# Performance work log

Measured on AMD Instinct MI355X. Metric: run time of the kernel, lower is better.

Reference implementation:

```python
import jax, jax.numpy as jnp
import numpy as np


def conv1x1(x, w, b):
    # x: (B,C,H,W), w: (Cout,Cin), b: (Cout,) -- 1x1 conv == channel matmul
    return jnp.einsum('bchw,oc->bohw', x, w) + b[None, :, None, None]


def spatial_gate(q_feat, k_feat, scale):
    # Faithful to: matmul over flattened (B*HW, C) x (C, B*HW), then
    # max over keys, mean over the batch axis, softmax over spatial dims.
    B, C, H, W = q_feat.shape
    q = q_feat.reshape(B, C, H * W).transpose(0, 2, 1).reshape(B * H * W, C)
    k = k_feat.reshape(B, C, H * W).transpose(1, 0, 2).reshape(C, B * H * W)
    s = (q @ k).reshape(B * H * W, B, H * W)          # (BHW, B, HW)
    m = jnp.mean(jnp.max(s, axis=-1), axis=-1)        # (BHW,)
    w = jax.nn.softmax(m.reshape(B, H * W) * scale, axis=-1)
    return w.reshape(B, 1, H, W)


def setup_inputs() -> dict:
    key = jax.random.key(0)
    ks = jax.random.split(key, 10)
    C = 256
    shp = (8, C, 32, 32)
    inp = {
        'x4': jax.random.normal(ks[0], shp, jnp.float32),
        'x3': jax.random.normal(ks[1], shp, jnp.float32),
        'wq': jax.random.normal(ks[2], (C, C), jnp.float32) * 0.02,
        'bq': jnp.zeros((C,), jnp.float32),
        'wk': jax.random.normal(ks[3], (C, C), jnp.float32) * 0.02,
        'bk': jnp.zeros((C,), jnp.float32),
        'wv': jax.random.normal(ks[4], (C, C), jnp.float32) * 0.02,
        'bv': jnp.zeros((C,), jnp.float32),
        'w128': jax.random.normal(ks[5], (128, C), jnp.float32) * 0.02,
        'b128': jnp.zeros((128,), jnp.float32),
    }
    return inp


def reference(x4, x3, wq, bq, wk, bk, wv, bv, w128, b128):
    C = x4.shape[1]
    scale = 1.0 / (C ** 0.5)
    # shared QKV 1x1 convs applied to both inputs
    aq = conv1x1(x4, wq, bq)
    ak = conv1x1(x4, wk, bk)
    av = conv1x1(x4, wv, bv)
    bq_f = conv1x1(x3, wq, bq)
    bk_f = conv1x1(x3, wk, bk)
    bv_f = conv1x1(x3, wv, bv)
    # four gating branches: self-self (a), self-self (b), cross a->b, cross b->a
    a_x4 = conv1x1(spatial_gate(aq, ak, scale) * av, w128, b128)
    b_x3 = conv1x1(spatial_gate(bq_f, bk_f, scale) * bv_f, w128, b128)
    x43 = conv1x1(spatial_gate(aq, bk_f, scale) * bv_f, w128, b128)
    x34 = conv1x1(spatial_gate(bq_f, ak, scale) * av, w128, b128)
    # cat order: [x34, a_x4] then [x43, b_x3]
    ab_cat = jnp.concatenate([x34, a_x4, x43, b_x3], axis=1)  # (B,512,H,W)
    # Block2D loop: block class undefined in source; surrogate = identity
    # (ab12 = concat of the two chunks == ab_cat), applied depth=4 times.
    ab12 = ab_cat
    ab12 = ab_cat * ab12
    ab_avg = jnp.mean(ab12, axis=(2, 3), keepdims=True)        # (B,512,1,1)
    ab = jax.nn.softmax(ab_avg, axis=-1)   # softmax over size-1 axis -> ones
    final = ab * ab_cat
    return final
```

## Files before the change

### kernel.cpp

```cpp
#include <hip/hip_runtime.h>

typedef unsigned short ushort_t;
typedef unsigned char uchar_t;
typedef __attribute__((ext_vector_type(8))) short bf16x8;
typedef __attribute__((ext_vector_type(4))) float f32x4;
typedef __attribute__((ext_vector_type(16))) float f32x16;
typedef __attribute__((ext_vector_type(8))) int v8i;

__device__ __forceinline__ unsigned short f2bf(float f) {
  union { float f; unsigned int u; } v; v.f = f;
  unsigned int r = v.u + 0x7FFFu + ((v.u >> 16) & 1u);
  return (unsigned short)(r >> 16);
}

__device__ __forceinline__ float bf2f(unsigned short u) {
  union { unsigned int i; float f; } v; v.i = ((unsigned int)u) << 16;
  return v.f;
}

__device__ __forceinline__ void gl_lds16(const void* gsrc, void* ldst) {
  __builtin_amdgcn_global_load_lds(
      (const __attribute__((address_space(1))) void*)gsrc,
      (__attribute__((address_space(3))) void*)ldst, 16, 0, 0);
}

__device__ __forceinline__ int frag_idx(int oc, int ci) {
  return (((oc>>4)*8 + (ci>>5))<<9) + ((((ci>>3)&3)*16 + (oc&15))<<3) + (ci&7);
}

__global__ __launch_bounds__(256) void k1_weights(
    const float* __restrict__ wq, const float* __restrict__ bq,
    const float* __restrict__ wk, const float* __restrict__ bk,
    const float* __restrict__ wv, const float* __restrict__ bv,
    const float* __restrict__ w128,
    ushort_t* __restrict__ Wf, float* __restrict__ bias_all)
{
  const int ci = threadIdx.x;
  const int oc = blockIdx.x;
  if (oc < 512) {
    const float v = (oc < 256) ? wq[oc*256 + ci] : wk[(oc-256)*256 + ci];
    Wf[frag_idx(oc, ci)] = f2bf(v);
    if (ci == 0) bias_all[oc] = (oc < 256) ? bq[oc] : bk[oc-256];
  } else {
    const int o = oc - 512;
    const float* wr = w128 + (size_t)o*256;
    float a = 0.f;
    for (int co = 0; co < 256; co++) a += wr[co] * wv[co*256 + ci];
    Wf[frag_idx(oc, ci)] = f2bf(a);
    if (ci == 0) {
      float s = 0.f;
      for (int co = 0; co < 256; co++) s += wr[co] * bv[co];
      bias_all[oc] = s;
    }
  }
}

__global__ __launch_bounds__(256) void k2_features(
    const float* __restrict__ x4, const float* __restrict__ x3,
    const ushort_t* __restrict__ Wf, const float* __restrict__ bias_all,
    uchar_t* __restrict__ Qf8, uchar_t* __restrict__ Kf8, float* __restrict__ V)
{
  __shared__ ushort_t Af[32*512];
  __shared__ ushort_t Wl[2][32*512];
  __shared__ ushort_t Lt[64*72];

  const int tid = threadIdx.x;
  const int w = tid >> 6, lane = tid & 63;
  const int mrow = lane & 15, quad = lane >> 4;
  const int ln31 = lane & 31, half = lane >> 5;

  const int px0 = blockIdx.x * 64;
  const int src = px0 >> 13, b = (px0 >> 10) & 7, hw0 = px0 & 1023;
  const float* xp = (src ? x3 : x4) + (size_t)b*262144;

  const int ot0 = blockIdx.y * 5;

  for (int kb = 0; kb < 8; kb++)
    gl_lds16(Wf + ((size_t)((ot0*4 + w)*8 + kb)<<9) + lane*8,
             &Wl[ot0&1][(w*8+kb)*512]);

  {
    const int hw = hw0 + w*16 + mrow;
    for (int kb = 0; kb < 8; kb++) {
      const int ch0 = kb*32 + quad*8;
      bf16x8 pk;
      #pragma unroll
      for (int j = 0; j < 8; j++)
        ((ushort_t*)&pk)[j] = f2bf(xp[(size_t)(ch0 + j)*1024 + hw]);
      *(bf16x8*)&Af[(w*8 + kb)*512 + lane*8] = pk;
    }
  }
  __syncthreads();

  for (int ot = ot0; ot < ot0 + 5; ot++) {
    const int nbuf = (ot+1) & 1, cbuf = ot & 1;
    if (ot + 1 < ot0 + 5) {
      for (int kb = 0; kb < 8; kb++)
        gl_lds16(Wf + ((size_t)(((ot+1)*4 + w)*8 + kb)<<9) + lane*8,
                 &Wl[nbuf][(w*8+kb)*512]);
      asm volatile("s_waitcnt vmcnt(32)" ::: "memory");
    } else {
      asm volatile("s_waitcnt vmcnt(0)" ::: "memory");
    }

    f32x4 acc[4];
    #pragma unroll
    for (int lg = 0; lg < 4; lg++) acc[lg] = (f32x4){0.f,0.f,0.f,0.f};
    #pragma unroll
    for (int kb = 0; kb < 8; kb++) {
      const bf16x8 a = *(const bf16x8*)&Wl[cbuf][(w*8 + kb)*512 + lane*8];
      #pragma unroll
      for (int lg = 0; lg < 4; lg++) {
        const bf16x8 bx = *(const bf16x8*)&Af[(lg*8 + kb)*512 + lane*8];
        acc[lg] = __builtin_amdgcn_mfma_f32_16x16x32_bf16(a, bx, acc[lg], 0, 0, 0);
      }
    }
    const int ocl = w*16 + quad*4;
    const float4 bias4 = *(const float4*)&bias_all[ot*64 + ocl];

    if (ot < 8) {
      __syncthreads();
      #pragma unroll
      for (int lg = 0; lg < 4; lg++) {
        const int px = lg*16 + mrow;
        ushort4 pk;
        pk.x = f2bf(acc[lg][0] + bias4.x);
        pk.y = f2bf(acc[lg][1] + bias4.y);
        pk.z = f2bf(acc[lg][2] + bias4.z);
        pk.w = f2bf(acc[lg][3] + bias4.w);
        *(ushort4*)&Lt[px*72 + ocl] = pk;
      }
      __syncthreads();
      const int g = w >> 1, e = w & 1;
      const int row = g*32 + ln31;
      const ushort_t* lp = &Lt[row*72 + e*32 + half*8];
      float fl[8], fh[8];
      #pragma unroll
      for (int j = 0; j < 8; j++) { fl[j] = bf2f(lp[j]); fh[j] = bf2f(lp[16+j]); }
      int w0 = __builtin_amdgcn_cvt_pk_fp8_f32(fl[0], fl[1], 0, 0);
      w0     = __builtin_amdgcn_cvt_pk_fp8_f32(fl[2], fl[3], w0, 1);
      int w1 = __builtin_amdgcn_cvt_pk_fp8_f32(fl[4], fl[5], 0, 0);
      w1     = __builtin_amdgcn_cvt_pk_fp8_f32(fl[6], fl[7], w1, 1);
      int w2 = __builtin_amdgcn_cvt_pk_fp8_f32(fh[0], fh[1], 0, 0);
      w2     = __builtin_amdgcn_cvt_pk_fp8_f32(fh[2], fh[3], w2, 1);
      int w3 = __builtin_amdgcn_cvt_pk_fp8_f32(fh[4], fh[5], 0, 0);
      w3     = __builtin_amdgcn_cvt_pk_fp8_f32(fh[6], fh[7], w3, 1);
      uchar_t* dst = (ot < 4) ? Qf8 : Kf8;
      const size_t chunk = (size_t)((px0>>5) + g)*8 + (ot&3)*2 + e;
      int4 pk4; pk4.x = w0; pk4.y = w1; pk4.z = w2; pk4.w = w3;
      *(int4*)(dst + (chunk<<10) + lane*16) = pk4;
    } else {
      const int ocv0 = (ot-8)*64 + ocl;
      float* vb = V + (((size_t)(src*8 + b)*128) << 10) + hw0;
      #pragma unroll
      for (int lg = 0; lg < 4; lg++) {
        vb[(size_t)(ocv0+0)*1024 + lg*16 + mrow] = acc[lg][0] + bias4.x;
        vb[(size_t)(ocv0+1)*1024 + lg*16 + mrow] = acc[lg][1] + bias4.y;
        vb[(size_t)(ocv0+2)*1024 + lg*16 + mrow] = acc[lg][2] + bias4.z;
        vb[(size_t)(ocv0+3)*1024 + lg*16 + mrow] = acc[lg][3] + bias4.w;
      }
    }
  }
}

__global__ __launch_bounds__(512, 2) void k3_smax(
    const uchar_t* __restrict__ Qf8, const uchar_t* __restrict__ Kf8,
    float* __restrict__ Pm)
{
  __shared__ __align__(16) uchar_t Kl[2][32768];

  const int tid = threadIdx.x;
  const int bt = blockIdx.x >> 5;
  const int rt = blockIdx.x & 31;
  const int w = tid >> 6, lane = tid & 63;
  const int ln31 = lane & 31, half = lane >> 5;

  const int rgb = rt*16 + w*2;
  const int ph = (blockIdx.x & 1)*4;

  #pragma unroll
  for (int q = 0; q < 4; q++) {
    const int c = w*4 + q;
    const int cg = bt*32 + ph*4 + (c>>3);
    gl_lds16(Kf8 + (((size_t)cg*8 + (c&7))<<10) + lane*16, &Kl[0][c*1024]);
  }

  v8i qa[2][4];
  #pragma unroll
  for (int rg = 0; rg < 2; rg++)
    #pragma unroll
    for (int u = 0; u < 4; u++) {
      const int4 p0 = *(const int4*)(Qf8 + (((size_t)(rgb + rg)*8 + 2*u+0)<<10) + lane*16);
      const int4 p1 = *(const int4*)(Qf8 + (((size_t)(rgb + rg)*8 + 2*u+1)<<10) + lane*16);
      qa[rg][u] = (v8i){p0.x, p0.y, p0.z, p0.w, p1.x, p1.y, p1.z, p1.w};
    }

  f32x16 zv;
  #pragma unroll
  for (int i = 0; i < 16; i++) zv[i] = 0.f;
  f32x16 rmax[2];
  #pragma unroll
  for (int rg = 0; rg < 2; rg++)
    #pragma unroll
    for (int i = 0; i < 16; i++) rmax[rg][i] = -3.4e38f;

  #pragma unroll 1
  for (int s = 0; s < 8; s++) {
    __syncthreads();
    if (s < 7) {
      const int sn = (s + 1 + ph) & 7;
      #pragma unroll
      for (int q = 0; q < 4; q++) {
        const int c = w*4 + q;
        const int cg = bt*32 + sn*4 + (c>>3);
        gl_lds16(Kf8 + (((size_t)cg*8 + (c&7))<<10) + lane*16,
                 &Kl[(s+1)&1][c*1024]);
      }
    }
    const uchar_t* kl = Kl[s & 1];

    int4 fA[8], fB[8];
    #pragma unroll
    for (int t = 0; t < 8; t++)
      fA[t] = *(const int4*)&kl[t*1024 + lane*16];

    #pragma unroll
    for (int cgl = 0; cgl < 4; cgl++) {
      if (cgl < 3) {
        #pragma unroll
        for (int t = 0; t < 8; t++)
          fB[t] = *(const int4*)&kl[((cgl+1)*8 + t)*1024 + lane*16];
      }
      f32x16 a0 = zv, a1 = zv;
      __builtin_amdgcn_s_setprio(1);
      #pragma unroll
      for (int u = 0; u < 4; u++) {
        const v8i bu = (v8i){fA[2*u].x,   fA[2*u].y,   fA[2*u].z,   fA[2*u].w,
                             fA[2*u+1].x, fA[2*u+1].y, fA[2*u+1].z, fA[2*u+1].w};
        a0 = __builtin_amdgcn_mfma_scale_f32_32x32x64_f8f6f4(
            qa[0][u], bu, a0, 0, 0, 0, 0x7F7F7F7F, 0, 0x7F7F7F7F);
        a1 = __builtin_amdgcn_mfma_scale_f32_32x32x64_f8f6f4(
            qa[1][u], bu, a1, 0, 0, 0, 0x7F7F7F7F, 0, 0x7F7F7F7F);
      }
      __builtin_amdgcn_s_setprio(0);
      #pragma unroll
      for (int i = 0; i < 16; i++) {
        rmax[0][i] = fmaxf(rmax[0][i], a0[i]);
        rmax[1][i] = fmaxf(rmax[1][i], a1[i]);
      }
      #pragma unroll
      for (int t = 0; t < 8; t++) fA[t] = fB[t];
    }
  }

  #pragma unroll
  for (int rg = 0; rg < 2; rg++) {
    #pragma unroll
    for (int e = 0; e < 16; e++) {
      float v = rmax[rg][e];
      v = fmaxf(v, __shfl_xor(v, 1));
      v = fmaxf(v, __shfl_xor(v, 2));
      v = fmaxf(v, __shfl_xor(v, 4));
      v = fmaxf(v, __shfl_xor(v, 8));
      v = fmaxf(v, __shfl_xor(v, 16));
      if (ln31 == 0) {
        const int row = rt*512 + w*64 + rg*32 + (e&3) + 8*(e>>2) + 4*half;
        Pm[(size_t)bt*16384 + row] = v;
      }
    }
  }
}

__global__ __launch_bounds__(256) void k5_out(
    const float* __restrict__ V, const float* __restrict__ Pm,
    const float* __restrict__ b128, float* __restrict__ out)
{
  __shared__ float xw[2][4];
  const int tid = threadIdx.x;
  const int ch = blockIdx.x & 511, b = blockIdx.x >> 9;
  const int blk = ch >> 7, o = ch & 127;
  const int gidx = (blk == 0) ? 2 : (blk == 1) ? 0 : (blk == 2) ? 1 : 3;
  const int src = (blk >= 2) ? 1 : 0;
  const int qset = gidx >> 1, side = gidx & 1;

  const float4* Pm4 = (const float4*)(Pm + (size_t)side*8*16384 + qset*8192 + b*1024);
  float4 l = {0.f, 0.f, 0.f, 0.f};
  #pragma unroll
  for (int t = 0; t < 8; t++) {
    const float4 p = Pm4[t*4096 + tid];
    l.x += p.x; l.y += p.y; l.z += p.z; l.w += p.w;
  }
  const float sc = 0.125f * 0.0625f;
  l.x *= sc; l.y *= sc; l.z *= sc; l.w *= sc;

  const int w = tid >> 6, lane = tid & 63;
  float m = fmaxf(fmaxf(l.x, l.y), fmaxf(l.z, l.w));
  #pragma unroll
  for (int d = 1; d < 64; d <<= 1) m = fmaxf(m, __shfl_xor(m, d));
  if (lane == 0) xw[0][w] = m;
  __syncthreads();
  m = fmaxf(fmaxf(xw[0][0], xw[0][1]), fmaxf(xw[0][2], xw[0][3]));

  float4 e;
  e.x = expf(l.x - m); e.y = expf(l.y - m);
  e.z = expf(l.z - m); e.w = expf(l.w - m);
  float s = e.x + e.y + e.z + e.w;
  #pragma unroll
  for (int d = 1; d < 64; d <<= 1) s += __shfl_xor(s, d);
  if (lane == 0) xw[1][w] = s;
  __syncthreads();
  s = xw[1][0] + xw[1][1] + xw[1][2] + xw[1][3];
  const float inv = 1.f / s;

  const int hw0 = tid << 2;
  const float4 v = *(const float4*)&V[((size_t)((src*8 + b)*128 + o) << 10) + hw0];
  const float bias = b128[o];
  float4 r;
  r.x = e.x*inv*v.x + bias; r.y = e.y*inv*v.y + bias;
  r.z = e.z*inv*v.z + bias; r.w = e.w*inv*v.w + bias;
  *(float4*)&out[((size_t)(b*512 + ch) << 10) + hw0] = r;
}

extern "C" void kernel_launch(void* const* d_in, const int* in_sizes, int n_in,
                              void* d_out, int out_size, void* d_ws, size_t ws_size,
                              hipStream_t stream)
{
  const float* x4   = (const float*)d_in[0];
  const float* x3   = (const float*)d_in[1];
  const float* wq   = (const float*)d_in[2];
  const float* bq   = (const float*)d_in[3];
  const float* wk   = (const float*)d_in[4];
  const float* bk   = (const float*)d_in[5];
  const float* wv   = (const float*)d_in[6];
  const float* bv   = (const float*)d_in[7];
  const float* w128 = (const float*)d_in[8];
  const float* b128 = (const float*)d_in[9];
  float* out = (float*)d_out;

  char* ws = (char*)d_ws;
  uchar_t*  Qf8 = (uchar_t*)ws;  ws += (size_t)512*8*1024;
  uchar_t*  Kf8 = (uchar_t*)ws;  ws += (size_t)512*8*1024;
  float*    V   = (float*)ws;    ws += (size_t)2*8*128*1024*4;
  float*    Pm  = (float*)ws;    ws += (size_t)16*16384*4;
  ushort_t* Wf  = (ushort_t*)ws; ws += (size_t)640*256*2;
  float* bias_all = (float*)ws;

  k1_weights <<<640,          256, 0, stream>>>(wq, bq, wk, bk, wv, bv, w128, Wf, bias_all);
  k2_features<<<dim3(256, 2), 256, 0, stream>>>(x4, x3, Wf, bias_all, Qf8, Kf8, V);
  k3_smax    <<<512,          512, 0, stream>>>(Qf8, Kf8, Pm);
  k5_out     <<<4096,         256, 0, stream>>>(V, Pm, b128, out);
}
```

Before: 181.8 us.

## Restructure score loop with manual barriers and deferred max reduction

Replaces the per-stage __syncthreads and register double-buffering of K fragments with explicit s_barrier/waitcnt placement inside each sub-chunk. The max reduction of the previous MFMA results is deferred so it overlaps with the next chunk's LDS loads, and the global-to-LDS prefetch is issued right after the first fragment loads. This is meant to let VALU max work and memory waits overlap the MFMA stream. The cost is more barriers per stage (two per sub-chunk), which could add synchronisation stalls.

```diff
diff --git a/kernel.cpp b/kernel.cpp
--- a/kernel.cpp
+++ b/kernel.cpp
@@ -204,53 +204,62 @@
     #pragma unroll
     for (int i = 0; i < 16; i++) rmax[rg][i] = -3.4e38f;
 
+  f32x16 fa0, fa1;
+  #pragma unroll
+  for (int i = 0; i < 16; i++) { fa0[i] = -3.4e38f; fa1[i] = -3.4e38f; }
+
+  asm volatile("s_waitcnt vmcnt(0)" ::: "memory");
+  __builtin_amdgcn_s_barrier();
+
   #pragma unroll 1
   for (int s = 0; s < 8; s++) {
-    __syncthreads();
-    if (s < 7) {
-      const int sn = (s + 1 + ph) & 7;
-      #pragma unroll
-      for (int q = 0; q < 4; q++) {
-        const int c = w*4 + q;
-        const int cg = bt*32 + sn*4 + (c>>3);
-        gl_lds16(Kf8 + (((size_t)cg*8 + (c&7))<<10) + lane*16,
-                 &Kl[(s+1)&1][c*1024]);
-      }
-    }
-    const uchar_t* kl = Kl[s & 1];
-
-    int4 fA[8], fB[8];
-    #pragma unroll
-    for (int t = 0; t < 8; t++)
-      fA[t] = *(const int4*)&kl[t*1024 + lane*16];
-
-    #pragma unroll
-    for (int cgl = 0; cgl < 4; cgl++) {
-      if (cgl < 3) {
+    const uchar_t* kl = &Kl[s & 1][0];
+    #pragma unroll
+    for (int c = 0; c < 4; c++) {
+      int4 fr[8];
+      #pragma unroll
+      for (int t = 0; t < 8; t++)
+        fr[t] = *(const int4*)&kl[(c*8 + t)*1024 + lane*16];
+      if (c == 0 && s < 7) {
+        const int sn = (s + 1 + ph) & 7;
         #pragma unroll
-        for (int t = 0; t < 8; t++)
-          fB[t] = *(const int4*)&kl[((cgl+1)*8 + t)*1024 + lane*16];
-      }
+        for (int q = 0; q < 4; q++) {
+          const int cc = w*4 + q;
+          const int cg = bt*32 + sn*4 + (cc>>3);
+          gl_lds16(Kf8 + (((size_t)cg*8 + (cc&7))<<10) + lane*16,
+                   &Kl[(s+1)&1][cc*1024]);
+        }
+      }
+      #pragma unroll
+      for (int i = 0; i < 16; i++) {
+        rmax[0][i] = fmaxf(rmax[0][i], fa0[i]);
+        rmax[1][i] = fmaxf(rmax[1][i], fa1[i]);
+      }
+      __builtin_amdgcn_s_barrier();
+      asm volatile("s_waitcnt lgkmcnt(0)" ::: "memory");
+      __builtin_amdgcn_sched_barrier(0);
       f32x16 a0 = zv, a1 = zv;
       __builtin_amdgcn_s_setprio(1);
       #pragma unroll
       for (int u = 0; u < 4; u++) {
-        const v8i bu = (v8i){fA[2*u].x,   fA[2*u].y,   fA[2*u].z,   fA[2*u].w,
-                             fA[2*u+1].x, fA[2*u+1].y, fA[2*u+1].z, fA[2*u+1].w};
+        const v8i bu = (v8i){fr[2*u].x,   fr[2*u].y,   fr[2*u].z,   fr[2*u].w,
+                             fr[2*u+1].x, fr[2*u+1].y, fr[2*u+1].z, fr[2*u+1].w};
         a0 = __builtin_amdgcn_mfma_scale_f32_32x32x64_f8f6f4(
             qa[0][u], bu, a0, 0, 0, 0, 0x7F7F7F7F, 0, 0x7F7F7F7F);
         a1 = __builtin_amdgcn_mfma_scale_f32_32x32x64_f8f6f4(
             qa[1][u], bu, a1, 0, 0, 0, 0x7F7F7F7F, 0, 0x7F7F7F7F);
       }
       __builtin_amdgcn_s_setprio(0);
-      #pragma unroll
-      for (int i = 0; i < 16; i++) {
-        rmax[0][i] = fmaxf(rmax[0][i], a0[i]);
-        rmax[1][i] = fmaxf(rmax[1][i], a1[i]);
-      }
-      #pragma unroll
-      for (int t = 0; t < 8; t++) fA[t] = fB[t];
-    }
+      fa0 = a0; fa1 = a1;
+      if (c == 3)
+        asm volatile("s_waitcnt vmcnt(0)" ::: "memory");
+      __builtin_amdgcn_s_barrier();
+    }
+  }
+  #pragma unroll
+  for (int i = 0; i < 16; i++) {
+    rmax[0][i] = fmaxf(rmax[0][i], fa0[i]);
+    rmax[1][i] = fmaxf(rmax[1][i], fa1[i]);
   }
 
   #pragma unroll
```

Result: no change. 184.6 us (+1.6%).
